# Kernel tuning notes

Measured on AMD Instinct MI355X. Metric: run time of the kernel, lower is better.

The kernel has to match this reference:

```python
import jax, jax.numpy as jnp
import numpy as np

NR, NS = 4, 3      # num_rotations, num_scales
RP, SP = 2, 2      # rotation_size, scale_size
K = 5              # kernel_size
PAD = 2
STRIDE = 1
NF = 9             # num basis functions (effective_size**2)


def setup_inputs() -> dict:
    key = jax.random.key(0)
    k1, k2, k3 = jax.random.split(key, 3)
    x = jax.random.normal(k1, (8, 16, NR * NS, 128, 128), dtype=jnp.float32)
    weight = jax.random.normal(k2, (16, 16, RP * SP, NF), dtype=jnp.float32) * 0.05
    basis = jax.random.normal(k3, (NF, NR * NS, K, K), dtype=jnp.float32)
    return {"x": x, "weight": weight, "basis": basis}


def reference(x, weight, basis):
    B, C, S, H, W = x.shape
    out_c, in_c, _, nf = weight.shape
    nrs = NR * NS
    # kernel synthesis: weight @ basis -> [nrs, out, in, RP*SP, K, K]
    kernel = jnp.einsum('oirf,fgxy->goirxy', weight, basis)
    kernel = kernel.reshape(nrs * out_c, in_c, RP, SP, K, K)
    # reshape input to [B, C, NR, NS, H, W]
    xg = x.reshape(B, C, NR, NS, H, W)
    # zero-pad scale axis at the end by SP-1
    xg = jnp.pad(xg, ((0, 0), (0, 0), (0, 0), (0, SP - 1), (0, 0), (0, 0)))
    # circular-pad rotation axis at the end by RP-1 (wrap from beginning)
    xg = jnp.concatenate([xg, xg[:, :, :RP - 1]], axis=2)
    out = None
    for i in range(RP):
        for j in range(SP):
            xs = xg[:, :, i:i + NR, j:j + NS]                     # [B,C,NR,NS,H,W]
            xs = xs.transpose(0, 2, 3, 1, 4, 5).reshape(B, nrs * C, H, W)
            o = jax.lax.conv_general_dilated(
                xs, kernel[:, :, i, j],
                window_strides=(STRIDE, STRIDE),
                padding=[(PAD, PAD), (PAD, PAD)],
                feature_group_count=nrs,
                dimension_numbers=('NCHW', 'OIHW', 'NCHW'))
            out = o if out is None else out + o
    B_, C_, H_, W_ = out.shape
    out = out.reshape(B_, nrs, out_c, H_, W_).transpose(0, 2, 1, 3, 4)
    return out
```

## Files before the change

kernel.cpp:

```cpp
#include <hip/hip_runtime.h>


#define NRS 12
#define CIN 16
#define COUT 16
#define HW 128
#define IMG (HW*HW)
#define ICSTRIDE (NRS*IMG)
#define HALO 36
#define NPIX (HALO*HALO)
#define HALFBYTES (NPIX*8*2)
#define ROWB (HALO*16)

typedef __bf16 bf16x8 __attribute__((ext_vector_type(8)));
typedef float  f32x4  __attribute__((ext_vector_type(4)));

__device__ __forceinline__ unsigned short f2bf(float f) {
    unsigned u = __builtin_bit_cast(unsigned, f);
    u += 0x7fffu + ((u >> 16) & 1u);
    return (unsigned short)(u >> 16);
}

__global__ void build_kc(const float* __restrict__ wgt, const float* __restrict__ basis,
                         unsigned short* __restrict__ kc) {
    int idx = blockIdx.x * 256 + threadIdx.x;
    const int total = 12 * 4 * 13 * 16 * 32;
    if (idx >= total) return;
    int k  = idx & 31;
    int possel = k >> 4, ic = k & 15;
    int o  = (idx >> 5) & 15;
    int t2 = idx >> 9;
    int pp = t2 % 13;
    int gr = t2 / 13;
    int rbase = gr & 3, g = gr >> 2;
    int pos = 2 * pp + possel;
    float s = 0.f;
    if (pos < 25) {
        int xk = pos / 5, yk = pos - 5 * xk;
        #pragma unroll
        for (int f = 0; f < 9; ++f)
            s = fmaf(wgt[((o * CIN + ic) * 4 + rbase) * 9 + f],
                     basis[((f * NRS + g) * 5 + xk) * 5 + yk], s);
    }
    kc[idx] = f2bf(s);
}

__global__ __launch_bounds__(256, 2)
void conv_mfma(const float* __restrict__ x, const unsigned short* __restrict__ kc,
               float* __restrict__ out) {
    const int b   = blockIdx.z;
    const int g   = blockIdx.y;
    const int th0 = (blockIdx.x >> 2) * 32;
    const int tw0 = (blockIdx.x & 3) * 32;
    const int r0 = g / 3, s0 = g - 3 * r0;

    const int t    = threadIdx.x;
    const int lane = t & 63;
    const int wave = t >> 6;
    const int n    = lane & 15;
    const int q    = lane >> 4;
    const int possel = q >> 1;
    const int half_  = q & 1;

    __shared__ uint4 xs4[(2 * HALFBYTES) / 16];
    char* xsc = (char*)xs4;

    int boff[13];
    #pragma unroll
    for (int pp = 0; pp < 13; ++pp) {
        int pos = 2 * pp + possel; if (pos > 24) pos = 24;
        int dx = pos / 5, dy = pos - 5 * dx;
        boff[pp] = half_ * HALFBYTES + dx * ROWB + (n + dy) * 16;
    }
    const int aoff = (lane & 15) * 32 + (lane >> 4) * 8;

    f32x4 acc[16];
    #pragma unroll
    for (int pg = 0; pg < 16; ++pg) acc[pg] = (f32x4){0.f, 0.f, 0.f, 0.f};

    for (int i = 0; i < 2; ++i) {
        int rr = r0 + i; if (rr >= 4) rr -= 4;
        for (int j = 0; j < 2; ++j) {
            int ss = s0 + j;
            if (ss >= 3) continue;
            const int sin_  = rr * 3 + ss;
            const int rbase = 2 * i + j;
            const float* xb = x + ((size_t)b * CIN * NRS + sin_) * IMG;

            __syncthreads();
            for (int p = t; p < NPIX; p += 256) {
                int rl = p / HALO, cl = p - rl * HALO;
                int hh = th0 + rl - 2, ww = tw0 + cl - 2;
                bool ok = ((unsigned)hh < 128u) && ((unsigned)ww < 128u);
                const float* px = xb + hh * HW + ww;
                unsigned short v[16];
                #pragma unroll
                for (int ic = 0; ic < 16; ++ic) {
                    float f = 0.f;
                    if (ok) f = px[(size_t)ic * ICSTRIDE];
                    v[ic] = f2bf(f);
                }
                uint4 lo, hi;
                lo.x = v[0] | (v[1] << 16);  lo.y = v[2] | (v[3] << 16);
                lo.z = v[4] | (v[5] << 16);  lo.w = v[6] | (v[7] << 16);
                hi.x = v[8] | (v[9] << 16);  hi.y = v[10] | (v[11] << 16);
                hi.z = v[12] | (v[13] << 16); hi.w = v[14] | (v[15] << 16);
                *(uint4*)(xsc + p * 16)             = lo;
                *(uint4*)(xsc + HALFBYTES + p * 16) = hi;
            }
            __syncthreads();

            const unsigned short* kcs = kc + (size_t)(g * 4 + rbase) * 13 * 512;
            const char* wb = xsc + wave * 8 * ROWB;
            #pragma unroll
            for (int pp = 0; pp < 13; ++pp) {
                bf16x8 af = *(const bf16x8*)(kcs + pp * 512 + aoff);
                const char* wp = wb + boff[pp];
                #pragma unroll
                for (int pg = 0; pg < 16; ++pg) {
                    bf16x8 bf = *(const bf16x8*)(wp + (pg >> 1) * ROWB + (pg & 1) * 256);
                    acc[pg] = __builtin_amdgcn_mfma_f32_16x16x32_bf16(af, bf, acc[pg], 0, 0, 0);
                }
            }
        }
    }

    const size_t obase = ((size_t)b * COUT * NRS + g) * IMG;
    #pragma unroll
    for (int pg = 0; pg < 16; ++pg) {
        int row = th0 + wave * 8 + (pg >> 1);
        int col = tw0 + (pg & 1) * 16 + n;
        size_t pix = (size_t)row * HW + col;
        #pragma unroll
        for (int r = 0; r < 4; ++r) {
            int o = q * 4 + r;
            out[obase + (size_t)o * NRS * IMG + pix] = acc[pg][r];
        }
    }
}

extern "C" void kernel_launch(void* const* d_in, const int* in_sizes, int n_in,
                              void* d_out, int out_size, void* d_ws, size_t ws_size,
                              hipStream_t stream) {
    const float* x      = (const float*)d_in[0];
    const float* weight = (const float*)d_in[1];
    const float* basis  = (const float*)d_in[2];
    float* out = (float*)d_out;
    unsigned short* kc = (unsigned short*)d_ws;

    build_kc<<<dim3((12 * 4 * 13 * 16 * 32 + 255) / 256), dim3(256), 0, stream>>>(weight, basis, kc);
    conv_mfma<<<dim3(16, NRS, 8), dim3(256), 0, stream>>>(x, kc, out);
}
```

Before: 283.0 us.

## Compute all three scale outputs per block to reuse staged input tiles

```diff
diff --git a/kernel.cpp b/kernel.cpp
--- a/kernel.cpp
+++ b/kernel.cpp
@@ -49,10 +49,9 @@
 void conv_mfma(const float* __restrict__ x, const unsigned short* __restrict__ kc,
                float* __restrict__ out) {
     const int b   = blockIdx.z;
-    const int g   = blockIdx.y;
+    const int r0  = blockIdx.y;
     const int th0 = (blockIdx.x >> 2) * 32;
     const int tw0 = (blockIdx.x & 3) * 32;
-    const int r0 = g / 3, s0 = g - 3 * r0;
 
     const int t    = threadIdx.x;
     const int lane = t & 63;
@@ -72,19 +71,20 @@
         int dx = pos / 5, dy = pos - 5 * dx;
         boff[pp] = half_ * HALFBYTES + dx * ROWB + (n + dy) * 16;
     }
-    const int aoff = (lane & 15) * 32 + (lane >> 4) * 8;
+    const int aoff = n * 32 + q * 8;
 
-    f32x4 acc[16];
+    f32x4 acc[3][16];
     #pragma unroll
-    for (int pg = 0; pg < 16; ++pg) acc[pg] = (f32x4){0.f, 0.f, 0.f, 0.f};
+    for (int s0 = 0; s0 < 3; ++s0)
+        #pragma unroll
+        for (int pg = 0; pg < 16; ++pg) acc[s0][pg] = (f32x4){0.f, 0.f, 0.f, 0.f};
 
+    #pragma unroll 1
     for (int i = 0; i < 2; ++i) {
         int rr = r0 + i; if (rr >= 4) rr -= 4;
-        for (int j = 0; j < 2; ++j) {
-            int ss = s0 + j;
-            if (ss >= 3) continue;
-            const int sin_  = rr * 3 + ss;
-            const int rbase = 2 * i + j;
+        #pragma unroll
+        for (int ss = 0; ss < 3; ++ss) {
+            const int sin_ = rr * 3 + ss;
             const float* xb = x + ((size_t)b * CIN * NRS + sin_) * IMG;
 
             __syncthreads();
@@ -110,31 +110,39 @@
             }
             __syncthreads();
 
-            const unsigned short* kcs = kc + (size_t)(g * 4 + rbase) * 13 * 512;
+            const unsigned short* kc0 = kc + (size_t)((r0 * 3 + ss) * 4 + 2 * i) * (13 * 512);
+            const unsigned short* kc1 = kc + (size_t)((r0 * 3 + ss - 1) * 4 + 2 * i + 1) * (13 * 512);
             const char* wb = xsc + wave * 8 * ROWB;
             #pragma unroll
             for (int pp = 0; pp < 13; ++pp) {
-                bf16x8 af = *(const bf16x8*)(kcs + pp * 512 + aoff);
+                bf16x8 af0 = *(const bf16x8*)(kc0 + pp * 512 + aoff);
+                bf16x8 af1;
+                if (ss > 0) af1 = *(const bf16x8*)(kc1 + pp * 512 + aoff);
                 const char* wp = wb + boff[pp];
                 #pragma unroll
                 for (int pg = 0; pg < 16; ++pg) {
-                    bf16x8 bf = *(const bf16x8*)(wp + (pg >> 1) * ROWB + (pg & 1) * 256);
-                    acc[pg] = __builtin_amdgcn_mfma_f32_16x16x32_bf16(af, bf, acc[pg], 0, 0, 0);
+                    bf16x8 bfv = *(const bf16x8*)(wp + (pg >> 1) * ROWB + (pg & 1) * 256);
+                    acc[ss][pg] = __builtin_amdgcn_mfma_f32_16x16x32_bf16(af0, bfv, acc[ss][pg], 0, 0, 0);
+                    if (ss > 0)
+                        acc[ss - 1][pg] = __builtin_amdgcn_mfma_f32_16x16x32_bf16(af1, bfv, acc[ss - 1][pg], 0, 0, 0);
                 }
             }
         }
     }
 
-    const size_t obase = ((size_t)b * COUT * NRS + g) * IMG;
     #pragma unroll
-    for (int pg = 0; pg < 16; ++pg) {
-        int row = th0 + wave * 8 + (pg >> 1);
-        int col = tw0 + (pg & 1) * 16 + n;
-        size_t pix = (size_t)row * HW + col;
+    for (int s0 = 0; s0 < 3; ++s0) {
+        const size_t obase = ((size_t)b * COUT * NRS + (r0 * 3 + s0)) * IMG;
         #pragma unroll
-        for (int r = 0; r < 4; ++r) {
-            int o = q * 4 + r;
-            out[obase + (size_t)o * NRS * IMG + pix] = acc[pg][r];
+        for (int pg = 0; pg < 16; ++pg) {
+            int row = th0 + wave * 8 + (pg >> 1);
+            int col = tw0 + (pg & 1) * 16 + n;
+            size_t pix = (size_t)row * HW + col;
+            #pragma unroll
+            for (int r = 0; r < 4; ++r) {
+                int o = q * 4 + r;
+                out[obase + (size_t)o * NRS * IMG + pix] = acc[s0][pg][r];
+            }
         }
     }
 }
@@ -149,5 +157,5 @@
     unsigned short* kc = (unsigned short*)d_ws;
 
     build_kc<<<dim3((12 * 4 * 13 * 16 * 32 + 255) / 256), dim3(256), 0, stream>>>(weight, basis, kc);
-    conv_mfma<<<dim3(16, NRS, 8), dim3(256), 0, stream>>>(x, kc, out);
+    conv_mfma<<<dim3(16, 4, 8), dim3(256), 0, stream>>>(x, kc, out);
 }
```

New measurement: 313.6 us. 1.11x slower.
